# Performance work log

Measured on AMD Instinct MI355X. Metric: run time of the kernel, lower is better.

## Reference

```python
import jax, jax.numpy as jnp
import numpy as np

NX, NY, NZ = 128, 128, 8
N_VOX = NX * NY * NZ
V, C, HF, WF = 6, 64, 116, 200
PAD_H, PAD_W = 928.0, 1600.0  # img_pad_shape (input image after padding)
IMG_H, IMG_W = 928.0, 1600.0  # img_shape used for the valid-flag bounds check


def _make_proj_mats():
    # Structured lidar2img matrices: pinhole intrinsics + 6 yaw-distributed cameras.
    K = np.array([[500.0, 0, 400, 0], [0, 500.0, 232, 0], [0, 0, 1, 0], [0, 0, 0, 1]], dtype=np.float64)
    A = np.array([[0.0, -1, 0], [0, 0, -1], [1, 0, 0]], dtype=np.float64)  # lidar(x fwd,y left,z up)->cam(z fwd)
    mats = []
    for j in range(V):
        yaw = 2.0 * np.pi * j / V
        c, s = np.cos(yaw), np.sin(yaw)
        Rz = np.array([[c, s, 0], [-s, c, 0], [0, 0, 1]])
        T = np.eye(4)
        T[:3, :3] = A @ Rz
        T[:3, 3] = np.array([0.0, -1.0, 0.0])
        mats.append(K @ T)
    return jnp.asarray(np.stack(mats), dtype=jnp.float32)


def setup_inputs() -> dict:
    key = jax.random.key(0)
    k1, k2 = jax.random.split(key)
    x_fov = jax.random.normal(k1, (1, V, C, HF, WF), dtype=jnp.float32)
    lo = jnp.array([-50.0, -50.0, -5.0], jnp.float32)
    span = jnp.array([100.0, 100.0, 8.0], jnp.float32)
    points = jax.random.uniform(k2, (N_VOX, 3), dtype=jnp.float32) * span + lo
    proj_mats = _make_proj_mats()
    return {"x_fov": x_fov, "points": points, "proj_mats": proj_mats}


def _bilinear_sample(feat, px, py):
    # feat [C,HF,WF]; px/py [N] in feature-map pixel coords.
    # Matches F.grid_sample(mode='bilinear', padding_mode='zeros', align_corners=False).
    x0 = jnp.floor(px)
    y0 = jnp.floor(py)
    wx1 = px - x0
    wy1 = py - y0

    def gather(xi, yi, w):
        inb = (xi >= 0) & (xi < WF) & (yi >= 0) & (yi < HF)
        xc = jnp.clip(xi, 0, WF - 1).astype(jnp.int32)
        yc = jnp.clip(yi, 0, HF - 1).astype(jnp.int32)
        return feat[:, yc, xc] * (w * inb)[None, :]  # [C,N]

    return (gather(x0, y0, (1 - wx1) * (1 - wy1))
            + gather(x0 + 1, y0, wx1 * (1 - wy1))
            + gather(x0, y0 + 1, (1 - wx1) * wy1)
            + gather(x0 + 1, y0 + 1, wx1 * wy1))


def _forward(x_fov, points, proj_mats):
    n = points.shape[0]
    # points_cam2img: homogeneous projection, perspective divide
    pts_h = jnp.concatenate([points, jnp.ones((n, 1), points.dtype)], axis=-1)  # [N,4]
    cam = jnp.einsum('vij,nj->vni', proj_mats, pts_h)  # [V,N,4]
    depth = cam[..., 2]
    d_safe = jnp.where(jnp.abs(depth) > 1e-6, depth, 1e-6)
    u = cam[..., 0] / d_safe  # image-plane x in input-image pixels (scale=1, crop=0, no flip)
    v = cam[..., 1] / d_safe
    # valid_flag: in front of camera and inside img_shape
    valid = (depth > 0) & (u > 0) & (u < IMG_W) & (v > 0) & (v < IMG_H)  # [V,N]
    # normalize by img_pad_shape then map to feature-map pixels (align_corners=False)
    px = u / PAD_W * WF - 0.5
    py = v / PAD_H * HF - 0.5
    feats = jax.vmap(_bilinear_sample)(x_fov[0], px, py)  # [V,C,N]
    feats = feats * valid[:, None, :].astype(feats.dtype)
    vol = feats.sum(0)  # [C,N] masked sum over views
    cnt = valid.sum(0).astype(feats.dtype)  # [N]
    vol = jnp.where(cnt > 0, vol, 0.0) / jnp.clip(cnt, 0.001)[None, :]
    # reshape(n_voxels[::-1] + [-1]).permute(3,2,1,0) -> [C,NX,NY,NZ]
    out = jnp.transpose(vol.reshape(C, NZ, NY, NX), (0, 3, 2, 1))
    return out[None]  # [1,C,NX,NY,NZ]


def reference(x_fov, points, proj_mats):
    return _forward(x_fov, points, proj_mats)
```

## Files before the change

### kernel.cpp

```cpp
#include <hip/hip_runtime.h>
#include <hip/hip_bf16.h>
#include <hip/hip_fp16.h>

#define NXv 128
#define NYv 128
#define NZv 8
#define NVOX (NXv * NYv * NZv)
#define NV 6
#define NC 64
#define HFv 116
#define WFv 200
#define PLANE (HFv * WFv)

#define FT_BYTES ((size_t)NV * PLANE * NC * 2)

typedef float v2f __attribute__((ext_vector_type(2)));

__device__ inline unsigned int f2bf(float f) {
  unsigned int x = __float_as_uint(f);
  unsigned int r = x + 0x7fffu + ((x >> 16) & 1u);
  return (r >> 16) & 0xffffu;
}
__device__ inline v2f bfpair(unsigned int u) {
  v2f r;
  r.x = __uint_as_float(u << 16);
  r.y = __uint_as_float(u & 0xffff0000u);
  return r;
}

__device__ inline unsigned short f2h_bits(float f) {
  __half h = __float2half(f);
  return *reinterpret_cast<unsigned short*>(&h);
}
__device__ inline float h_bits2f(unsigned short u) {
  __half_raw r; r.x = u;
  __half h = *reinterpret_cast<__half*>(&r);
  return __half2float(h);
}

__global__ __launch_bounds__(256) void transpose_feat_bf16(
    const float* __restrict__ in, unsigned int* __restrict__ out32) {
  __shared__ float tile[64][65];
  const int v  = blockIdx.y;
  const int p0 = blockIdx.x * 64;
  const float* src = in + (size_t)v * NC * PLANE;
  unsigned int* dst = out32 + (size_t)v * PLANE * (NC / 2);
  const int t = threadIdx.x;

#pragma unroll
  for (int i = 0; i < 4; ++i) {
    const int idx = i * 256 + t;
    const int c  = idx >> 4;
    const int p4 = idx & 15;
    const int pp = p0 + p4 * 4;
    if (pp < PLANE) {
      const float4 f = *(const float4*)(src + (size_t)c * PLANE + pp);
      tile[p4 * 4 + 0][c] = f.x;
      tile[p4 * 4 + 1][c] = f.y;
      tile[p4 * 4 + 2][c] = f.z;
      tile[p4 * 4 + 3][c] = f.w;
    }
  }
  __syncthreads();

#pragma unroll
  for (int i = 0; i < 2; ++i) {
    const int idx = i * 256 + t;
    const int p   = idx >> 3;
    const int c8  = idx & 7;
    const int pp  = p0 + p;
    if (pp < PLANE) {
      uint4 w;
      w.x = f2bf(tile[p][c8 * 8 + 0]) | (f2bf(tile[p][c8 * 8 + 1]) << 16);
      w.y = f2bf(tile[p][c8 * 8 + 2]) | (f2bf(tile[p][c8 * 8 + 3]) << 16);
      w.z = f2bf(tile[p][c8 * 8 + 4]) | (f2bf(tile[p][c8 * 8 + 5]) << 16);
      w.w = f2bf(tile[p][c8 * 8 + 6]) | (f2bf(tile[p][c8 * 8 + 7]) << 16);
      *(uint4*)(dst + (size_t)pp * 32 + c8 * 4) = w;
    }
  }
}

__global__ __launch_bounds__(256, 4) void gather_fused(
    const uint4* __restrict__ feat4,
    const float* __restrict__ points,
    const float* __restrict__ proj,
    float* __restrict__ out) {
  __shared__ uint2  pdl_pix[64][NV];
  __shared__ float4 pdl_w[64][NV];
  __shared__ unsigned short tile_h[64][66];
  __shared__ unsigned int vmask[64];
  __shared__ float projl[96];

  const int bi   = blockIdx.x;
  const int xcd  = bi & 7;
  const int r    = bi >> 3;
  const int tid  = xcd * 2 + (r >> 7);
  const int q    = r & 127;
  const int ix   = (tid & 3) * 32 + (q & 31);
  const int iyg  = (tid >> 2) * 4 + (q >> 5);
  const int iy0g = iyg * 8;

  const int t    = threadIdx.x;
  const int lane = t & 63;
  const int wave = t >> 6;

  if (t < 96) projl[t] = proj[t];
  if (t < 64) vmask[t] = 0u;
  __syncthreads();

  {
    const int slot = t & 63;
    const int vb   = t >> 6;
    const int j    = slot >> 3;
    const int iz   = slot & 7;
    const int n    = iz * (NXv * NYv) + (iy0g + j) * NXv + ix;

    const float x = points[n * 3 + 0];
    const float y = points[n * 3 + 1];
    const float z = points[n * 3 + 2];

#pragma unroll
    for (int vo = 0; vo < 2; ++vo) {
      const int v = vb + vo * 4;
      if (v < NV) {
        const float* M = projl + v * 16;
        const float cx = M[0] * x + M[1] * y + M[2]  * z + M[3];
        const float cy = M[4] * x + M[5] * y + M[6]  * z + M[7];
        const float cz = M[8] * x + M[9] * y + M[10] * z + M[11];

        const float dz = (fabsf(cz) > 1e-6f) ? cz : 1e-6f;
        const float u  = cx / dz;
        const float vv = cy / dz;

        const bool valid = (cz > 0.0f) && (u > 0.0f) && (u < 1600.0f) &&
                           (vv > 0.0f) && (vv < 928.0f);
        if (valid) {
          const float px = u  / 1600.0f * 200.0f - 0.5f;
          const float py = vv / 928.0f  * 116.0f - 0.5f;
          const float fx0 = floorf(px);
          const float fy0 = floorf(py);
          const float wx1 = px - fx0;
          const float wy1 = py - fy0;
          const float wx0 = 1.0f - wx1;
          const float wy0 = 1.0f - wy1;
          const int ix0 = (int)fx0;
          const int iy0 = (int)fy0;

          const bool bx0 = (ix0 >= 0) && (ix0 < WFv);
          const bool bx1 = (ix0 + 1 >= 0) && (ix0 + 1 < WFv);
          const bool by0 = (iy0 >= 0) && (iy0 < HFv);
          const bool by1 = (iy0 + 1 >= 0) && (iy0 + 1 < HFv);

          const int xc0 = min(max(ix0, 0), WFv - 1);
          const int xc1 = min(max(ix0 + 1, 0), WFv - 1);
          const int yc0 = min(max(iy0, 0), HFv - 1);
          const int yc1 = min(max(iy0 + 1, 0), HFv - 1);
          const unsigned int p00 = (unsigned int)(yc0 * WFv + xc0);
          const unsigned int p10 = (unsigned int)(yc0 * WFv + xc1);
          const unsigned int p01 = (unsigned int)(yc1 * WFv + xc0);
          const unsigned int p11 = (unsigned int)(yc1 * WFv + xc1);

          uint2 pix;
          pix.x = p00 | (p10 << 16);
          pix.y = p01 | (p11 << 16);
          float4 wv;
          wv.x = (bx0 && by0) ? wx0 * wy0 : 0.0f;
          wv.y = (bx1 && by0) ? wx1 * wy0 : 0.0f;
          wv.z = (bx0 && by1) ? wx0 * wy1 : 0.0f;
          wv.w = (bx1 && by1) ? wx1 * wy1 : 0.0f;
          pdl_pix[slot][v] = pix;
          pdl_w[slot][v]   = wv;
          atomicOr(&vmask[slot], 1u << v);
        } else {
          pdl_pix[slot][v] = (uint2){0u, 0u};
          pdl_w[slot][v]   = (float4){0.0f, 0.0f, 0.0f, 0.0f};
        }
      }
    }
  }
  __syncthreads();

  const int pg2  = lane >> 4;
  const int ch   = (lane >> 1) & 7;
  const int half = lane & 1;

#pragma unroll
  for (int i = 0; i < 4; ++i) {
    const int gi = wave * 4 + i;
    const int jg = gi >> 3;
    const int iz = gi & 7;
    const int sl = (jg * 4 + pg2) * 8 + iz;

    const unsigned int m0 = vmask[sl];
    const int mycnt = __popc(m0);
    const int vdead = min(__builtin_ctz(~m0), NV - 1);

    int km = mycnt;
    km = max(km, __shfl_xor(km, 16));
    km = max(km, __shfl_xor(km, 32));

    v2f acc2[4];
#pragma unroll
    for (int j2 = 0; j2 < 4; ++j2) acc2[j2] = (v2f){0.0f, 0.0f};

    unsigned int m = m0;
    for (int k = 0; k < km; ++k) {
      const bool live = (k < mycnt);
      const int v = live ? __builtin_ctz(m | 0x40u) : vdead;
      m &= m - 1;

      const uint2 pix = pdl_pix[sl][v];
      const unsigned int ui = half ? pix.y : pix.x;
      const unsigned int pa = ui & 0xffffu;
      const unsigned int pb = ui >> 16;
      const v2f wp = *((const v2f*)&pdl_w[sl][v] + half);

      const uint4* fb = feat4 + (size_t)v * (PLANE * 8) + ch;
      const uint4 qa = fb[(size_t)pa * 8];
      const uint4 qb = fb[(size_t)pb * 8];

      const v2f wva = (v2f){wp.x, wp.x};
      const v2f wvb = (v2f){wp.y, wp.y};

      acc2[0] = __builtin_elementwise_fma(wva, bfpair(qa.x), acc2[0]);
      acc2[1] = __builtin_elementwise_fma(wva, bfpair(qa.y), acc2[1]);
      acc2[2] = __builtin_elementwise_fma(wva, bfpair(qa.z), acc2[2]);
      acc2[3] = __builtin_elementwise_fma(wva, bfpair(qa.w), acc2[3]);

      acc2[0] = __builtin_elementwise_fma(wvb, bfpair(qb.x), acc2[0]);
      acc2[1] = __builtin_elementwise_fma(wvb, bfpair(qb.y), acc2[1]);
      acc2[2] = __builtin_elementwise_fma(wvb, bfpair(qb.z), acc2[2]);
      acc2[3] = __builtin_elementwise_fma(wvb, bfpair(qb.w), acc2[3]);
    }

#pragma unroll
    for (int j2 = 0; j2 < 4; ++j2) {
      acc2[j2].x += __shfl_xor(acc2[j2].x, 1);
      acc2[j2].y += __shfl_xor(acc2[j2].y, 1);
    }

    if (half == 0) {
      const float inv = (mycnt > 0) ? 1.0f / (float)mycnt : 0.0f;
#pragma unroll
      for (int j2 = 0; j2 < 4; ++j2) {
        const unsigned int pk =
            (unsigned int)f2h_bits(acc2[j2].x * inv) |
            ((unsigned int)f2h_bits(acc2[j2].y * inv) << 16);
        *(unsigned int*)&tile_h[sl][ch * 8 + j2 * 2] = pk;
      }
    }
  }

  __syncthreads();

  const size_t obase = (size_t)ix * (NYv * NZv) + (size_t)iy0g * NZv + lane;
#pragma unroll
  for (int i = 0; i < 16; ++i) {
    const int c = i * 4 + wave;
    const float val = h_bits2f(tile_h[lane][c]);
    __builtin_nontemporal_store(val, &out[(size_t)c * NVOX + obase]);
  }
}

__global__ __launch_bounds__(256) void sample_fallback(
    const float* __restrict__ feat,
    const float* __restrict__ points,
    const float* __restrict__ proj,
    float* __restrict__ out) {
  const int wave = threadIdx.x >> 6;
  const int lane = threadIdx.x & 63;
  const int n = blockIdx.x * 4 + wave;

  const float x = points[n * 3 + 0];
  const float y = points[n * 3 + 1];
  const float z = points[n * 3 + 2];

  float acc = 0.0f;
  int cnt = 0;

#pragma unroll
  for (int v = 0; v < NV; ++v) {
    const float* M = proj + v * 16;
    const float cx = M[0] * x + M[1] * y + M[2]  * z + M[3];
    const float cy = M[4] * x + M[5] * y + M[6]  * z + M[7];
    const float cz = M[8] * x + M[9] * y + M[10] * z + M[11];
    const float dz = (fabsf(cz) > 1e-6f) ? cz : 1e-6f;
    const float u  = cx / dz;
    const float vv = cy / dz;
    const bool valid = (cz > 0.0f) && (u > 0.0f) && (u < 1600.0f) &&
                       (vv > 0.0f) && (vv < 928.0f);
    if (!valid) continue;
    cnt++;
    const float px = u  / 1600.0f * 200.0f - 0.5f;
    const float py = vv / 928.0f  * 116.0f - 0.5f;
    const float fx0 = floorf(px);
    const float fy0 = floorf(py);
    const float wx1 = px - fx0;
    const float wy1 = py - fy0;
    const float wx0 = 1.0f - wx1;
    const float wy0 = 1.0f - wy1;
    const int ix0 = (int)fx0;
    const int iy0 = (int)fy0;
    const float w00 = wx0 * wy0, w10 = wx1 * wy0, w01 = wx0 * wy1, w11 = wx1 * wy1;
    const float* basev = feat + ((size_t)v * NC + lane) * PLANE;
    auto tap = [&](int xi, int yi, float w) {
      if (xi >= 0 && xi < WFv && yi >= 0 && yi < HFv)
        acc += w * basev[yi * WFv + xi];
    };
    tap(ix0,     iy0,     w00);
    tap(ix0 + 1, iy0,     w10);
    tap(ix0,     iy0 + 1, w01);
    tap(ix0 + 1, iy0 + 1, w11);
  }

  const float scale = (cnt > 0) ? (1.0f / (float)cnt) : 0.0f;
  const int iz  = n >> 14;
  const int rem = n & 16383;
  const int iy  = rem >> 7;
  const int ixx = rem & 127;
  out[(((size_t)lane * NXv + ixx) * NYv + iy) * NZv + iz] = acc * scale;
}

extern "C" void kernel_launch(void* const* d_in, const int* in_sizes, int n_in,
                              void* d_out, int out_size, void* d_ws, size_t ws_size,
                              hipStream_t stream) {
  const float* x_fov  = (const float*)d_in[0];
  const float* points = (const float*)d_in[1];
  const float* proj   = (const float*)d_in[2];
  float* out = (float*)d_out;

  if (ws_size >= FT_BYTES) {
    unsigned int* ft = (unsigned int*)d_ws;
    dim3 tgrid((PLANE + 63) / 64, NV);
    transpose_feat_bf16<<<tgrid, 256, 0, stream>>>(x_fov, ft);
    gather_fused<<<NXv * NYv / 8, 256, 0, stream>>>((const uint4*)ft, points, proj, out);
  } else {
    sample_fallback<<<NVOX / 4, 256, 0, stream>>>(x_fov, points, proj, out);
  }
}
```

Baseline: 100.5 us.

## Fuse feature transpose and gather into one cooperative kernel with grid sync

Adds a cooperative kernel that first computes per-voxel projections and bilinear weights into shared memory. It then runs a grid-strided bf16 transpose of the feature maps and does a grid-wide sync before the gather phase. The goal is to remove the second kernel launch and its gap, and to overlap projection math with the transpose. The risk is grid-sync overhead and lower occupancy. The path is used only when the occupancy query reports at least 8 resident blocks per CU; otherwise it falls back to the two-kernel path.

```diff
diff --git a/kernel.cpp b/kernel.cpp
--- a/kernel.cpp
+++ b/kernel.cpp
@@ -1,6 +1,9 @@
 #include <hip/hip_runtime.h>
+#include <hip/hip_cooperative_groups.h>
 #include <hip/hip_bf16.h>
 #include <hip/hip_fp16.h>
+
+namespace cg = cooperative_groups;
 
 #define NXv 128
 #define NYv 128
@@ -11,6 +14,8 @@
 #define HFv 116
 #define WFv 200
 #define PLANE (HFv * WFv)
+#define K1_TILES 2178
+#define COOP_GRID 2048
 
 #define FT_BYTES ((size_t)NV * PLANE * NC * 2)
 
@@ -37,6 +42,7 @@
   __half h = *reinterpret_cast<__half*>(&r);
   return __half2float(h);
 }
+
 
 __global__ __launch_bounds__(256) void transpose_feat_bf16(
     const float* __restrict__ in, unsigned int* __restrict__ out32) {
@@ -179,6 +185,239 @@
     }
   }
   __syncthreads();
+
+  const int pg2  = lane >> 4;
+  const int ch   = (lane >> 1) & 7;
+  const int half = lane & 1;
+
+#pragma unroll
+  for (int i = 0; i < 4; ++i) {
+    const int gi = wave * 4 + i;
+    const int jg = gi >> 3;
+    const int iz = gi & 7;
+    const int sl = (jg * 4 + pg2) * 8 + iz;
+
+    const unsigned int m0 = vmask[sl];
+    const int mycnt = __popc(m0);
+    const int vdead = min(__builtin_ctz(~m0), NV - 1);
+
+    int km = mycnt;
+    km = max(km, __shfl_xor(km, 16));
+    km = max(km, __shfl_xor(km, 32));
+
+    v2f acc2[4];
+#pragma unroll
+    for (int j2 = 0; j2 < 4; ++j2) acc2[j2] = (v2f){0.0f, 0.0f};
+
+    unsigned int m = m0;
+    for (int k = 0; k < km; ++k) {
+      const bool live = (k < mycnt);
+      const int v = live ? __builtin_ctz(m | 0x40u) : vdead;
+      m &= m - 1;
+
+      const uint2 pix = pdl_pix[sl][v];
+      const unsigned int ui = half ? pix.y : pix.x;
+      const unsigned int pa = ui & 0xffffu;
+      const unsigned int pb = ui >> 16;
+      const v2f wp = *((const v2f*)&pdl_w[sl][v] + half);
+
+      const uint4* fb = feat4 + (size_t)v * (PLANE * 8) + ch;
+      const uint4 qa = fb[(size_t)pa * 8];
+      const uint4 qb = fb[(size_t)pb * 8];
+
+      const v2f wva = (v2f){wp.x, wp.x};
+      const v2f wvb = (v2f){wp.y, wp.y};
+
+      acc2[0] = __builtin_elementwise_fma(wva, bfpair(qa.x), acc2[0]);
+      acc2[1] = __builtin_elementwise_fma(wva, bfpair(qa.y), acc2[1]);
+      acc2[2] = __builtin_elementwise_fma(wva, bfpair(qa.z), acc2[2]);
+      acc2[3] = __builtin_elementwise_fma(wva, bfpair(qa.w), acc2[3]);
+
+      acc2[0] = __builtin_elementwise_fma(wvb, bfpair(qb.x), acc2[0]);
+      acc2[1] = __builtin_elementwise_fma(wvb, bfpair(qb.y), acc2[1]);
+      acc2[2] = __builtin_elementwise_fma(wvb, bfpair(qb.z), acc2[2]);
+      acc2[3] = __builtin_elementwise_fma(wvb, bfpair(qb.w), acc2[3]);
+    }
+
+#pragma unroll
+    for (int j2 = 0; j2 < 4; ++j2) {
+      acc2[j2].x += __shfl_xor(acc2[j2].x, 1);
+      acc2[j2].y += __shfl_xor(acc2[j2].y, 1);
+    }
+
+    if (half == 0) {
+      const float inv = (mycnt > 0) ? 1.0f / (float)mycnt : 0.0f;
+#pragma unroll
+      for (int j2 = 0; j2 < 4; ++j2) {
+        const unsigned int pk =
+            (unsigned int)f2h_bits(acc2[j2].x * inv) |
+            ((unsigned int)f2h_bits(acc2[j2].y * inv) << 16);
+        *(unsigned int*)&tile_h[sl][ch * 8 + j2 * 2] = pk;
+      }
+    }
+  }
+
+  __syncthreads();
+
+  const size_t obase = (size_t)ix * (NYv * NZv) + (size_t)iy0g * NZv + lane;
+#pragma unroll
+  for (int i = 0; i < 16; ++i) {
+    const int c = i * 4 + wave;
+    const float val = h_bits2f(tile_h[lane][c]);
+    __builtin_nontemporal_store(val, &out[(size_t)c * NVOX + obase]);
+  }
+}
+
+__global__ __launch_bounds__(256, 4) void fused_coop(
+    const float* __restrict__ x_fov,
+    unsigned int* __restrict__ ft,
+    const float* __restrict__ points,
+    const float* __restrict__ proj,
+    float* __restrict__ out) {
+  __shared__ float projl[96];
+  __shared__ unsigned int vmask[64];
+  __shared__ uint2 pdl_pix[64][NV];
+  __shared__ float4 pdl_w[64][NV];
+  __shared__ __align__(16) unsigned char scratch[8448];
+
+  const int bi   = blockIdx.x;
+  const int t    = threadIdx.x;
+  const int lane = t & 63;
+  const int wave = t >> 6;
+
+  const int xcd  = bi & 7;
+  const int r    = bi >> 3;
+  const int tid  = xcd * 2 + (r >> 7);
+  const int q    = r & 127;
+  const int ix   = (tid & 3) * 32 + (q & 31);
+  const int iyg  = (tid >> 2) * 4 + (q >> 5);
+  const int iy0g = iyg * 8;
+
+  if (t < 96) projl[t] = proj[t];
+  if (t < 64) vmask[t] = 0u;
+  __syncthreads();
+
+  {
+    const int slot = t & 63;
+    const int vb   = t >> 6;
+    const int j    = slot >> 3;
+    const int iz   = slot & 7;
+    const int n    = iz * (NXv * NYv) + (iy0g + j) * NXv + ix;
+
+    const float x = points[n * 3 + 0];
+    const float y = points[n * 3 + 1];
+    const float z = points[n * 3 + 2];
+
+#pragma unroll
+    for (int vo = 0; vo < 2; ++vo) {
+      const int v = vb + vo * 4;
+      if (v < NV) {
+        const float* M = projl + v * 16;
+        const float cx = M[0] * x + M[1] * y + M[2]  * z + M[3];
+        const float cy = M[4] * x + M[5] * y + M[6]  * z + M[7];
+        const float cz = M[8] * x + M[9] * y + M[10] * z + M[11];
+
+        const float dz = (fabsf(cz) > 1e-6f) ? cz : 1e-6f;
+        const float u  = cx / dz;
+        const float vv = cy / dz;
+
+        const bool valid = (cz > 0.0f) && (u > 0.0f) && (u < 1600.0f) &&
+                           (vv > 0.0f) && (vv < 928.0f);
+        if (valid) {
+          const float px = u  / 1600.0f * 200.0f - 0.5f;
+          const float py = vv / 928.0f  * 116.0f - 0.5f;
+          const float fx0 = floorf(px);
+          const float fy0 = floorf(py);
+          const float wx1 = px - fx0;
+          const float wy1 = py - fy0;
+          const float wx0 = 1.0f - wx1;
+          const float wy0 = 1.0f - wy1;
+          const int ix0 = (int)fx0;
+          const int iy0 = (int)fy0;
+
+          const bool bx0 = (ix0 >= 0) && (ix0 < WFv);
+          const bool bx1 = (ix0 + 1 >= 0) && (ix0 + 1 < WFv);
+          const bool by0 = (iy0 >= 0) && (iy0 < HFv);
+          const bool by1 = (iy0 + 1 >= 0) && (iy0 + 1 < HFv);
+
+          const int xc0 = min(max(ix0, 0), WFv - 1);
+          const int xc1 = min(max(ix0 + 1, 0), WFv - 1);
+          const int yc0 = min(max(iy0, 0), HFv - 1);
+          const int yc1 = min(max(iy0 + 1, 0), HFv - 1);
+          const unsigned int p00 = (unsigned int)(yc0 * WFv + xc0);
+          const unsigned int p10 = (unsigned int)(yc0 * WFv + xc1);
+          const unsigned int p01 = (unsigned int)(yc1 * WFv + xc0);
+          const unsigned int p11 = (unsigned int)(yc1 * WFv + xc1);
+
+          uint2 pix;
+          pix.x = p00 | (p10 << 16);
+          pix.y = p01 | (p11 << 16);
+          float4 wv;
+          wv.x = (bx0 && by0) ? wx0 * wy0 : 0.0f;
+          wv.y = (bx1 && by0) ? wx1 * wy0 : 0.0f;
+          wv.z = (bx0 && by1) ? wx0 * wy1 : 0.0f;
+          wv.w = (bx1 && by1) ? wx1 * wy1 : 0.0f;
+          pdl_pix[slot][v] = pix;
+          pdl_w[slot][v]   = wv;
+          atomicOr(&vmask[slot], 1u << v);
+        } else {
+          pdl_pix[slot][v] = (uint2){0u, 0u};
+          pdl_w[slot][v]   = (float4){0.0f, 0.0f, 0.0f, 0.0f};
+        }
+      }
+    }
+  }
+  __syncthreads();
+
+  {
+    float (*tile)[65] = (float(*)[65])scratch;
+    for (int tl = bi; tl < K1_TILES; tl += COOP_GRID) {
+      const int v  = tl / 363;
+      const int tp = tl - v * 363;
+      const float* src = x_fov + (size_t)v * NC * PLANE;
+      unsigned int* dst = ft + (size_t)v * PLANE * 32;
+
+#pragma unroll
+      for (int h = 0; h < 2; ++h) {
+        const int p0 = tp * 64 + h * 32;
+#pragma unroll
+        for (int i = 0; i < 2; ++i) {
+          const int idx = i * 256 + t;
+          const int c  = idx >> 3;
+          const int p4 = idx & 7;
+          const int pp = p0 + p4 * 4;
+          if (pp < PLANE) {
+            const float4 f = *(const float4*)(src + (size_t)c * PLANE + pp);
+            tile[p4 * 4 + 0][c] = f.x;
+            tile[p4 * 4 + 1][c] = f.y;
+            tile[p4 * 4 + 2][c] = f.z;
+            tile[p4 * 4 + 3][c] = f.w;
+          }
+        }
+        __syncthreads();
+        {
+          const int p  = t >> 3;
+          const int c8 = t & 7;
+          const int pp = p0 + p;
+          if (pp < PLANE) {
+            uint4 w;
+            w.x = f2bf(tile[p][c8 * 8 + 0]) | (f2bf(tile[p][c8 * 8 + 1]) << 16);
+            w.y = f2bf(tile[p][c8 * 8 + 2]) | (f2bf(tile[p][c8 * 8 + 3]) << 16);
+            w.z = f2bf(tile[p][c8 * 8 + 4]) | (f2bf(tile[p][c8 * 8 + 5]) << 16);
+            w.w = f2bf(tile[p][c8 * 8 + 6]) | (f2bf(tile[p][c8 * 8 + 7]) << 16);
+            *(uint4*)(dst + (size_t)pp * 32 + c8 * 4) = w;
+          }
+        }
+        __syncthreads();
+      }
+    }
+  }
+
+  __threadfence();
+  cg::this_grid().sync();
+
+  const uint4* feat4 = (const uint4*)ft;
+  unsigned short (*tile_h)[66] = (unsigned short(*)[66])scratch;
 
   const int pg2  = lane >> 4;
   const int ch   = (lane >> 1) & 7;
@@ -331,6 +570,25 @@
 
   if (ws_size >= FT_BYTES) {
     unsigned int* ft = (unsigned int*)d_ws;
+
+    static int coop_state = -1;
+    if (coop_state == -1) {
+      int nb = 0;
+      hipError_t qe = hipOccupancyMaxActiveBlocksPerMultiprocessor(
+          &nb, (const void*)fused_coop, 256, 0);
+      coop_state = (qe == hipSuccess && nb >= 8) ? 1 : 0;
+    }
+
+    if (coop_state == 1) {
+      void* args[] = {(void*)&x_fov, (void*)&ft, (void*)&points,
+                      (void*)&proj, (void*)&out};
+      hipError_t le = hipLaunchCooperativeKernel(
+          (const void*)fused_coop, dim3(COOP_GRID), dim3(256), args, 0, stream);
+      if (le == hipSuccess) return;
+      (void)hipGetLastError();
+      coop_state = 0;
+    }
+
     dim3 tgrid((PLANE + 63) / 64, NV);
     transpose_feat_bf16<<<tgrid, 256, 0, stream>>>(x_fov, ft);
     gather_fused<<<NXv * NYv / 8, 256, 0, stream>>>((const uint4*)ft, points, proj, out);
```

New measurement: 100.6 us. Within noise of the previous version (+0.1%).
